# Performance work log

Measured on AMD Instinct MI355X. Metric: run time of the kernel, lower is better.

Reference implementation:

```python
import jax, jax.numpy as jnp
import numpy as np

B, D, H = 1024, 128, 128
LN_EPS = 1e-5


def setup_inputs() -> dict:
    key = jax.random.key(0)
    ks = jax.random.split(key, 12)
    s_d = 1.0 / np.sqrt(D)
    s_h = 1.0 / np.sqrt(H)
    return {
        "x": jax.random.normal(ks[0], (B, D), dtype=jnp.float32),
        # diff_proj: Linear(D, H)
        "Wd": jax.random.uniform(ks[1], (H, D), jnp.float32, -s_d, s_d),
        "bd": jax.random.uniform(ks[2], (H,), jnp.float32, -s_d, s_d),
        # tau_proj: Linear(D, 1) -> Softplus
        "Wt": jax.random.uniform(ks[3], (1, D), jnp.float32, -s_d, s_d),
        "bt": jax.random.uniform(ks[4], (1,), jnp.float32, -s_d, s_d),
        # agg: Linear(H, H) -> ReLU
        "Wa": jax.random.uniform(ks[5], (H, H), jnp.float32, -s_h, s_h),
        "ba": jax.random.uniform(ks[6], (H,), jnp.float32, -s_h, s_h),
        # res_proj: Linear(D, H)
        "Wr": jax.random.uniform(ks[7], (H, D), jnp.float32, -s_d, s_d),
        "br": jax.random.uniform(ks[8], (H,), jnp.float32, -s_d, s_d),
        # LayerNorm(H)
        "gamma": jnp.ones((H,), jnp.float32),
        "beta": jnp.zeros((H,), jnp.float32),
    }


def reference(x, Wd, bd, Wt, bt, Wa, ba, Wr, br, gamma, beta):
    # mean_j diff_proj(|x_i - x_j|) == diff_proj(mean_j |x_i - x_j|) since Linear is affine
    diffs_mean = jnp.mean(jnp.abs(x[:, None, :] - x[None, :, :]), axis=1)  # [B, D]
    d_mean = diffs_mean @ Wd.T + bd                                         # [B, H]
    # tau = softplus(x Wt^T + bt).clamp(min=0.01) + 1.0
    tau = jnp.clip(jax.nn.softplus(x @ Wt.T + bt), 0.01, None) + 1.0        # [B, 1]
    h_mean = d_mean / tau
    h = jax.nn.relu(h_mean @ Wa.T + ba)
    y = h + x @ Wr.T + br
    mu = jnp.mean(y, axis=-1, keepdims=True)
    var = jnp.var(y, axis=-1, keepdims=True)
    return (y - mu) / jnp.sqrt(var + LN_EPS) * gamma + beta
```

## Files before the change

### kernel.cpp

```cpp
#include <hip/hip_runtime.h>
#include <math.h>

#define Bn 1024
#define Dn 128
#define Hn 128

__global__ __launch_bounds__(256) void fused_resd1(
    const float* __restrict__ x,
    const float* __restrict__ Wd, const float* __restrict__ bd,
    const float* __restrict__ Wt, const float* __restrict__ bt,
    const float* __restrict__ Wa, const float* __restrict__ ba,
    const float* __restrict__ Wr, const float* __restrict__ br,
    const float* __restrict__ gamma, const float* __restrict__ beta,
    float* __restrict__ out) {
  const int t = threadIdx.x;
  const int d = t & 127;
  const int g = t >> 7;
  const int i0 = blockIdx.x << 2;

  __shared__ float xs[4][Dn];
  __shared__ float dms[4][Dn];
  __shared__ float ms[4][Hn];
  __shared__ float ys[4][Hn];
  __shared__ float red[4][Dn];
  __shared__ float wt_s[Dn];
  __shared__ float tau_s[4];

  const float xi0 = x[(i0 + 0) * Dn + d];
  const float xi1 = x[(i0 + 1) * Dn + d];
  const float xi2 = x[(i0 + 2) * Dn + d];
  const float xi3 = x[(i0 + 3) * Dn + d];
  float a0 = 0.f, a1 = 0.f, a2 = 0.f, a3 = 0.f;
  const float* xp = x + (size_t)g * 512 * Dn + d;
#pragma unroll 1
  for (int j = 0; j < 512; j += 8) {
    float xj[8];
#pragma unroll
    for (int u = 0; u < 8; ++u) xj[u] = xp[(j + u) * Dn];
#pragma unroll
    for (int u = 0; u < 8; ++u) {
      a0 += fabsf(xi0 - xj[u]);
      a1 += fabsf(xi1 - xj[u]);
      a2 += fabsf(xi2 - xj[u]);
      a3 += fabsf(xi3 - xj[u]);
    }
  }

  if (g == 0) {
    red[0][d] = a0; red[1][d] = a1; red[2][d] = a2; red[3][d] = a3;
    xs[0][d] = xi0; xs[1][d] = xi1; xs[2][d] = xi2; xs[3][d] = xi3;
    wt_s[d] = Wt[d];
  }
  __syncthreads();
  if (g == 1) {
    const float s = 1.0f / 1024.0f;
    dms[0][d] = (red[0][d] + a0) * s;
    dms[1][d] = (red[1][d] + a1) * s;
    dms[2][d] = (red[2][d] + a2) * s;
    dms[3][d] = (red[3][d] + a3) * s;
  }
  __syncthreads();

  {
    const int r = t >> 6, p = t & 63;
    float partial = xs[r][p] * wt_s[p] + xs[r][p + 64] * wt_s[p + 64];
#pragma unroll
    for (int off = 32; off; off >>= 1) partial += __shfl_xor(partial, off, 64);
    if (p == 0) {
      const float z = partial + bt[0];
      const float sp = fmaxf(z, 0.f) + log1pf(expf(-fabsf(z)));
      tau_s[r] = 1.0f / (fmaxf(sp, 0.01f) + 1.0f);
    }
  }
  __syncthreads();

  const int h = d;
  const int r0 = 2 * g, r1 = 2 * g + 1;
  {
    float m0 = bd[h], m1 = m0;
    const float4* w = (const float4*)(Wd + (size_t)h * Dn);
#pragma unroll 4
    for (int k4 = 0; k4 < Dn / 4; ++k4) {
      const float4 wv = w[k4];
      const int k = k4 * 4;
      m0 += wv.x * dms[r0][k] + wv.y * dms[r0][k + 1] + wv.z * dms[r0][k + 2] + wv.w * dms[r0][k + 3];
      m1 += wv.x * dms[r1][k] + wv.y * dms[r1][k + 1] + wv.z * dms[r1][k + 2] + wv.w * dms[r1][k + 3];
    }
    ms[r0][h] = m0 * tau_s[r0];
    ms[r1][h] = m1 * tau_s[r1];
  }
  __syncthreads();

  {
    float q0 = ba[h], q1 = q0, c0 = br[h], c1 = c0;
    const float4* wa = (const float4*)(Wa + (size_t)h * Dn);
    const float4* wr = (const float4*)(Wr + (size_t)h * Dn);
#pragma unroll 4
    for (int k4 = 0; k4 < Dn / 4; ++k4) {
      const float4 av = wa[k4];
      const float4 rv = wr[k4];
      const int k = k4 * 4;
      q0 += av.x * ms[r0][k] + av.y * ms[r0][k + 1] + av.z * ms[r0][k + 2] + av.w * ms[r0][k + 3];
      q1 += av.x * ms[r1][k] + av.y * ms[r1][k + 1] + av.z * ms[r1][k + 2] + av.w * ms[r1][k + 3];
      c0 += rv.x * xs[r0][k] + rv.y * xs[r0][k + 1] + rv.z * xs[r0][k + 2] + rv.w * xs[r0][k + 3];
      c1 += rv.x * xs[r1][k] + rv.y * xs[r1][k + 1] + rv.z * xs[r1][k + 2] + rv.w * xs[r1][k + 3];
    }
    ys[r0][h] = fmaxf(q0, 0.f) + c0;
    ys[r1][h] = fmaxf(q1, 0.f) + c1;
  }
  __syncthreads();

  {
    const int r = t >> 6, p = t & 63;
    const float v0 = ys[r][p], v1 = ys[r][p + 64];
    float s = v0 + v1;
    float q = v0 * v0 + v1 * v1;
#pragma unroll
    for (int off = 32; off; off >>= 1) {
      s += __shfl_xor(s, off, 64);
      q += __shfl_xor(q, off, 64);
    }
    const float mu = s * (1.0f / 128.0f);
    const float var = q * (1.0f / 128.0f) - mu * mu;
    const float rs = rsqrtf(var + 1e-5f);
    float* o = out + (size_t)(i0 + r) * Hn;
    o[p]      = (v0 - mu) * rs * gamma[p]      + beta[p];
    o[p + 64] = (v1 - mu) * rs * gamma[p + 64] + beta[p + 64];
  }
}

extern "C" void kernel_launch(void* const* d_in, const int* in_sizes, int n_in,
                              void* d_out, int out_size, void* d_ws, size_t ws_size,
                              hipStream_t stream) {
  const float* x     = (const float*)d_in[0];
  const float* Wd    = (const float*)d_in[1];
  const float* bd    = (const float*)d_in[2];
  const float* Wt    = (const float*)d_in[3];
  const float* bt    = (const float*)d_in[4];
  const float* Wa    = (const float*)d_in[5];
  const float* ba    = (const float*)d_in[6];
  const float* Wr    = (const float*)d_in[7];
  const float* br    = (const float*)d_in[8];
  const float* gamma = (const float*)d_in[9];
  const float* beta  = (const float*)d_in[10];
  float* out = (float*)d_out;

  fused_resd1<<<Bn / 4, 256, 0, stream>>>(x, Wd, bd, Wt, bt, Wa, ba, Wr, br,
                                          gamma, beta, out);
  (void)in_sizes; (void)n_in; (void)out_size; (void)d_ws; (void)ws_size;
}
```

Baseline: 109.8 us.

## Split pairwise abs-diff reduction across 32 warps with float4 loads

Raises the block from 256 to 1024 threads. Each group of 32 lanes handles 32 j-rows using float4 vector loads across all 128 features, instead of 2 groups each scanning 512 rows serially. Partial sums go into a 64KB shared buffer and are then reduced across the 32 groups. This shortens the serial per-thread chain in the dominant O(B^2 D) phase, at the cost of much more shared memory, which limits blocks per CU, and of leaving 3/4 of the threads idle in the later GEMV and LayerNorm phases.

```diff
diff --git a/kernel.cpp b/kernel.cpp
--- a/kernel.cpp
+++ b/kernel.cpp
@@ -5,7 +5,7 @@
 #define Dn 128
 #define Hn 128
 
-__global__ __launch_bounds__(256) void fused_resd1(
+__global__ __launch_bounds__(1024) void fused_resd1(
     const float* __restrict__ x,
     const float* __restrict__ Wd, const float* __restrict__ bd,
     const float* __restrict__ Wt, const float* __restrict__ bt,
@@ -14,54 +14,61 @@
     const float* __restrict__ gamma, const float* __restrict__ beta,
     float* __restrict__ out) {
   const int t = threadIdx.x;
-  const int d = t & 127;
-  const int g = t >> 7;
+  const int c = t & 31;
+  const int g = t >> 5;
   const int i0 = blockIdx.x << 2;
 
+  __shared__ float red[32][4][Dn];
   __shared__ float xs[4][Dn];
   __shared__ float dms[4][Dn];
   __shared__ float ms[4][Hn];
   __shared__ float ys[4][Hn];
-  __shared__ float red[4][Dn];
   __shared__ float wt_s[Dn];
   __shared__ float tau_s[4];
 
-  const float xi0 = x[(i0 + 0) * Dn + d];
-  const float xi1 = x[(i0 + 1) * Dn + d];
-  const float xi2 = x[(i0 + 2) * Dn + d];
-  const float xi3 = x[(i0 + 3) * Dn + d];
-  float a0 = 0.f, a1 = 0.f, a2 = 0.f, a3 = 0.f;
-  const float* xp = x + (size_t)g * 512 * Dn + d;
+  float4 xi[4];
+#pragma unroll
+  for (int r = 0; r < 4; ++r)
+    xi[r] = *(const float4*)(x + (size_t)(i0 + r) * Dn + c * 4);
+
+  float4 acc[4];
+#pragma unroll
+  for (int r = 0; r < 4; ++r) acc[r] = make_float4(0.f, 0.f, 0.f, 0.f);
+
+  const float4* xq = (const float4*)x + (size_t)g * 32 * (Dn / 4) + c;
 #pragma unroll 1
-  for (int j = 0; j < 512; j += 8) {
-    float xj[8];
+  for (int jj = 0; jj < 32; jj += 4) {
+    float4 xj[4];
 #pragma unroll
-    for (int u = 0; u < 8; ++u) xj[u] = xp[(j + u) * Dn];
+    for (int u = 0; u < 4; ++u) xj[u] = xq[(size_t)(jj + u) * (Dn / 4)];
 #pragma unroll
-    for (int u = 0; u < 8; ++u) {
-      a0 += fabsf(xi0 - xj[u]);
-      a1 += fabsf(xi1 - xj[u]);
-      a2 += fabsf(xi2 - xj[u]);
-      a3 += fabsf(xi3 - xj[u]);
+    for (int u = 0; u < 4; ++u) {
+#pragma unroll
+      for (int r = 0; r < 4; ++r) {
+        acc[r].x += fabsf(xi[r].x - xj[u].x);
+        acc[r].y += fabsf(xi[r].y - xj[u].y);
+        acc[r].z += fabsf(xi[r].z - xj[u].z);
+        acc[r].w += fabsf(xi[r].w - xj[u].w);
+      }
     }
   }
+#pragma unroll
+  for (int r = 0; r < 4; ++r) *(float4*)&red[g][r][c * 4] = acc[r];
+  __syncthreads();
 
-  if (g == 0) {
-    red[0][d] = a0; red[1][d] = a1; red[2][d] = a2; red[3][d] = a3;
-    xs[0][d] = xi0; xs[1][d] = xi1; xs[2][d] = xi2; xs[3][d] = xi3;
-    wt_s[d] = Wt[d];
-  }
-  __syncthreads();
-  if (g == 1) {
-    const float s = 1.0f / 1024.0f;
-    dms[0][d] = (red[0][d] + a0) * s;
-    dms[1][d] = (red[1][d] + a1) * s;
-    dms[2][d] = (red[2][d] + a2) * s;
-    dms[3][d] = (red[3][d] + a3) * s;
+  if (t < 512) {
+    const int r = t >> 7, d = t & 127;
+    float s = 0.f;
+#pragma unroll
+    for (int gg = 0; gg < 32; ++gg) s += red[gg][r][d];
+    dms[r][d] = s * (1.0f / 1024.0f);
+    xs[r][d] = x[(size_t)(i0 + r) * Dn + d];
+  } else if (t < 640) {
+    wt_s[t - 512] = Wt[t - 512];
   }
   __syncthreads();
 
-  {
+  if (t < 256) {
     const int r = t >> 6, p = t & 63;
     float partial = xs[r][p] * wt_s[p] + xs[r][p + 64] * wt_s[p + 64];
 #pragma unroll
@@ -74,9 +81,10 @@
   }
   __syncthreads();
 
-  const int h = d;
-  const int r0 = 2 * g, r1 = 2 * g + 1;
-  {
+  if (t < 256) {
+    const int h = t & 127;
+    const int g4 = t >> 7;
+    const int r0 = 2 * g4, r1 = 2 * g4 + 1;
     float m0 = bd[h], m1 = m0;
     const float4* w = (const float4*)(Wd + (size_t)h * Dn);
 #pragma unroll 4
@@ -91,7 +99,10 @@
   }
   __syncthreads();
 
-  {
+  if (t < 256) {
+    const int h = t & 127;
+    const int g4 = t >> 7;
+    const int r0 = 2 * g4, r1 = 2 * g4 + 1;
     float q0 = ba[h], q1 = q0, c0 = br[h], c1 = c0;
     const float4* wa = (const float4*)(Wa + (size_t)h * Dn);
     const float4* wr = (const float4*)(Wr + (size_t)h * Dn);
@@ -110,7 +121,7 @@
   }
   __syncthreads();
 
-  {
+  if (t < 256) {
     const int r = t >> 6, p = t & 63;
     const float v0 = ys[r][p], v1 = ys[r][p + 64];
     float s = v0 + v1;
@@ -145,7 +156,7 @@
   const float* beta  = (const float*)d_in[10];
   float* out = (float*)d_out;
 
-  fused_resd1<<<Bn / 4, 256, 0, stream>>>(x, Wd, bd, Wt, bt, Wa, ba, Wr, br,
-                                          gamma, beta, out);
+  fused_resd1<<<Bn / 4, 1024, 0, stream>>>(x, Wd, bd, Wt, bt, Wa, ba, Wr, br,
+                                           gamma, beta, out);
   (void)in_sizes; (void)n_in; (void)out_size; (void)d_ws; (void)ws_size;
 }
```

Result: faster. 96.46 us (-12.2%).
